# Kernel optimization log

Measured on AMD Instinct MI355X. Metric: run time of the kernel, lower is better.

## Reference

```python
import jax, jax.numpy as jnp
import numpy as np

ROUTINGS = 3
NUM_CAPSULE = 32
DIM_CAPSULE = 32
EPS_KERAS = 1e-7   # K.epsilon()
EPS_L2 = 1e-12     # tf.nn.l2_normalize epsilon


def squash(x, axis=-1):
    s2 = jnp.sum(jnp.square(x), axis=axis, keepdims=True)
    return (s2 / (1.0 + s2)) * x / jnp.sqrt(s2 + EPS_KERAS)


def l2_normalize(x, axis=-1):
    s2 = jnp.sum(jnp.square(x), axis=axis, keepdims=True)
    return x * jax.lax.rsqrt(jnp.maximum(s2, EPS_L2))


def setup_inputs() -> dict:
    key = jax.random.key(0)
    k1, k2 = jax.random.split(key)
    u_vecs = jax.random.normal(k1, (32, 2048, 16), dtype=jnp.float32)
    # glorot-like small scale for the local kernel to keep routing numerics sane
    W = jax.random.normal(k2, (2048, 16, NUM_CAPSULE * DIM_CAPSULE), dtype=jnp.float32) * 0.05
    return {"u_vecs": u_vecs, "W": W}


def reference(u_vecs, W):
    B, N_in, _ = u_vecs.shape
    # local_conv1d with kernel size 1 == per-input-capsule matmul
    u_hat = jnp.einsum('bni,nio->bno', u_vecs, W)
    # [B, N_in, num_cap, dim] -> [B, num_cap, N_in, dim]
    u_hat = u_hat.reshape(B, N_in, NUM_CAPSULE, DIM_CAPSULE).transpose(0, 2, 1, 3)
    b = jnp.zeros((B, NUM_CAPSULE, N_in), dtype=u_hat.dtype)
    o = None
    for i in range(ROUTINGS):
        c = jax.nn.softmax(b, axis=1)              # softmax over output capsules
        o = jnp.einsum('bin,binj->bij', c, u_hat)  # [B, num_cap, dim]
        if i < ROUTINGS - 1:
            o = l2_normalize(o, axis=-1)
            b = jnp.einsum('bij,binj->bin', o, u_hat)
    return squash(o, axis=-1)
```

## Files before the change

### kernel.cpp

```cpp
#include <hip/hip_runtime.h>
#include <math.h>
#include <stdint.h>

#define BB   32
#define NN   2048
#define KK   16
#define CC   32
#define DD   32
#define NCOL 1024
#define NPB  8
#define WT   (KK * NCOL)
#define OSZ  (BB * NCOL)
#define NGRP (NN / NPB)
#define NSLICE 8

__global__ __launch_bounds__(512) __attribute__((amdgpu_waves_per_eu(2)))
void caps_stage(const float* __restrict__ u, const float* __restrict__ W,
                const float* __restrict__ onorm, float* __restrict__ part)
{
    __shared__ float ush[NPB * KK * BB];

    const int tid  = threadIdx.x;
    const int wv   = tid >> 6;
    const int lane = tid & 63;
    const int oct  = lane >> 3;
    const int dq   = lane & 7;
    const int b0   = wv << 2;
    const int n0   = blockIdx.x * NPB;

    for (int idx = tid; idx < NPB * KK * BB; idx += 512) {
        const int k = idx & 15, b = (idx >> 4) & 31, n = idx >> 9;
        ush[(n << 9) + (k << 5) + b] =
            u[(size_t)b * (NN * KK) + (size_t)(n0 + n) * KK + k];
    }
    __syncthreads();

    const float* wp = W + (size_t)n0 * WT + (lane << 2);

    float opart[4][4][4];
#pragma unroll
    for (int b = 0; b < 4; ++b)
#pragma unroll
        for (int j = 0; j < 4; ++j)
#pragma unroll
            for (int e = 0; e < 4; ++e) opart[b][j][e] = 0.f;

    for (int nn = 0; nn < NPB; ++nn) {
        const float* un = &ush[nn << 9];

        float accU[4][4][4];
#pragma unroll
        for (int b = 0; b < 4; ++b)
#pragma unroll
            for (int j = 0; j < 4; ++j)
#pragma unroll
                for (int e = 0; e < 4; ++e) accU[b][j][e] = 0.f;

#pragma unroll
        for (int k = 0; k < KK; ++k) {
            const float4 w0 = *(const float4*)(wp + k * NCOL);
            const float4 w1 = *(const float4*)(wp + k * NCOL + 256);
            const float4 w2 = *(const float4*)(wp + k * NCOL + 512);
            const float4 w3 = *(const float4*)(wp + k * NCOL + 768);
            const float4 ub = *(const float4*)&un[(k << 5) + b0];
            const float us[4] = {ub.x, ub.y, ub.z, ub.w};
#pragma unroll
            for (int b = 0; b < 4; ++b) {
                accU[b][0][0] = fmaf(us[b], w0.x, accU[b][0][0]);
                accU[b][0][1] = fmaf(us[b], w0.y, accU[b][0][1]);
                accU[b][0][2] = fmaf(us[b], w0.z, accU[b][0][2]);
                accU[b][0][3] = fmaf(us[b], w0.w, accU[b][0][3]);
                accU[b][1][0] = fmaf(us[b], w1.x, accU[b][1][0]);
                accU[b][1][1] = fmaf(us[b], w1.y, accU[b][1][1]);
                accU[b][1][2] = fmaf(us[b], w1.z, accU[b][1][2]);
                accU[b][1][3] = fmaf(us[b], w1.w, accU[b][1][3]);
                accU[b][2][0] = fmaf(us[b], w2.x, accU[b][2][0]);
                accU[b][2][1] = fmaf(us[b], w2.y, accU[b][2][1]);
                accU[b][2][2] = fmaf(us[b], w2.z, accU[b][2][2]);
                accU[b][2][3] = fmaf(us[b], w2.w, accU[b][2][3]);
                accU[b][3][0] = fmaf(us[b], w3.x, accU[b][3][0]);
                accU[b][3][1] = fmaf(us[b], w3.y, accU[b][3][1]);
                accU[b][3][2] = fmaf(us[b], w3.z, accU[b][3][2]);
                accU[b][3][3] = fmaf(us[b], w3.w, accU[b][3][3]);
            }
        }
        wp += WT;

        float cv[4][4];
#pragma unroll
        for (int b = 0; b < 4; ++b) {
            float L[4];
#pragma unroll
            for (int j = 0; j < 4; ++j) {
                const float4 on4 = *(const float4*)(
                    onorm + ((size_t)(b0 + b) * CC + oct + (j << 3)) * DD + (dq << 2));
                float p = accU[b][j][0] * on4.x + accU[b][j][1] * on4.y
                        + accU[b][j][2] * on4.z + accU[b][j][3] * on4.w;
                p += __shfl_xor(p, 1);
                p += __shfl_xor(p, 2);
                p += __shfl_xor(p, 4);
                L[j] = p;
            }
            float mx = fmaxf(fmaxf(L[0], L[1]), fmaxf(L[2], L[3]));
            mx = fmaxf(mx, __shfl_xor(mx, 8));
            mx = fmaxf(mx, __shfl_xor(mx, 16));
            mx = fmaxf(mx, __shfl_xor(mx, 32));
            float s = 0.f;
#pragma unroll
            for (int j = 0; j < 4; ++j) { L[j] = __expf(L[j] - mx); s += L[j]; }
            s += __shfl_xor(s, 8);
            s += __shfl_xor(s, 16);
            s += __shfl_xor(s, 32);
            const float inv = 1.f / s;
#pragma unroll
            for (int j = 0; j < 4; ++j) cv[b][j] = L[j] * inv;
        }

#pragma unroll
        for (int b = 0; b < 4; ++b)
#pragma unroll
            for (int j = 0; j < 4; ++j)
#pragma unroll
                for (int e = 0; e < 4; ++e)
                    opart[b][j][e] = fmaf(cv[b][j], accU[b][j][e], opart[b][j][e]);
    }

    float* my = part + (size_t)blockIdx.x * OSZ + (size_t)b0 * NCOL + (lane << 2);
#pragma unroll
    for (int b = 0; b < 4; ++b)
#pragma unroll
        for (int j = 0; j < 4; ++j) {
            float4 v;
            v.x = opart[b][j][0]; v.y = opart[b][j][1];
            v.z = opart[b][j][2]; v.w = opart[b][j][3];
            *(float4*)&my[b * NCOL + (j << 8)] = v;
        }
}

__global__ __launch_bounds__(256) void caps_reduce1(
    const float* __restrict__ part, float* __restrict__ ws2)
{
    const int gid   = blockIdx.x * 256 + threadIdx.x;
    const int slice = gid >> 13;
    const int q     = gid & 8191;
    float4 acc = make_float4(0.f, 0.f, 0.f, 0.f);
    const float* p = part + ((size_t)slice * 32) * OSZ + (q << 2);
#pragma unroll 8
    for (int j = 0; j < 32; ++j) {
        const float4 v = *(const float4*)(p + (size_t)j * OSZ);
        acc.x += v.x; acc.y += v.y; acc.z += v.z; acc.w += v.w;
    }
    *(float4*)(ws2 + ((size_t)gid << 2)) = acc;
}

__global__ __launch_bounds__(256) void caps_reduce2(
    const float* __restrict__ ws2, float* __restrict__ dst, int mode)
{
    const int q = blockIdx.x * 256 + threadIdx.x;
    float4 acc = make_float4(0.f, 0.f, 0.f, 0.f);
#pragma unroll
    for (int s = 0; s < NSLICE; ++s) {
        const float4 v = *(const float4*)(ws2 + ((size_t)s << 15) + (q << 2));
        acc.x += v.x; acc.y += v.y; acc.z += v.z; acc.w += v.w;
    }
    float s2 = acc.x * acc.x + acc.y * acc.y + acc.z * acc.z + acc.w * acc.w;
    s2 += __shfl_xor(s2, 1);
    s2 += __shfl_xor(s2, 2);
    s2 += __shfl_xor(s2, 4);
    float scale;
    if (mode == 0) {
        scale = rsqrtf(fmaxf(s2, 1e-12f));
    } else {
        scale = (s2 / (1.f + s2)) / sqrtf(s2 + 1e-7f);
    }
    float4 o;
    o.x = acc.x * scale; o.y = acc.y * scale;
    o.z = acc.z * scale; o.w = acc.w * scale;
    *(float4*)(dst + ((size_t)q << 2)) = o;
}

extern "C" void kernel_launch(void* const* d_in, const int* in_sizes, int n_in,
                              void* d_out, int out_size, void* d_ws, size_t ws_size,
                              hipStream_t stream)
{
    const float* u = (const float*)d_in[0];
    const float* W = (const float*)d_in[1];
    float* out = (float*)d_out;

    float* part  = (float*)d_ws;
    float* ws2   = part + (size_t)NGRP * OSZ;
    float* onorm = ws2 + (size_t)NSLICE * OSZ;

    hipMemsetAsync(onorm, 0, (size_t)OSZ * sizeof(float), stream);

    for (int it = 0; it < 3; ++it) {
        caps_stage<<<NGRP, 512, 0, stream>>>(u, W, onorm, part);
        caps_reduce1<<<256, 256, 0, stream>>>(part, ws2);
        if (it < 2)
            caps_reduce2<<<32, 256, 0, stream>>>(ws2, onorm, 0);
        else
            caps_reduce2<<<32, 256, 0, stream>>>(ws2, out, 1);
    }
}
```

Measured before the change: 410.6 us.

## Split batch across two block halves to double grid size in caps stage

```diff
diff --git a/kernel.cpp b/kernel.cpp
--- a/kernel.cpp
+++ b/kernel.cpp
@@ -3,6 +3,7 @@
 #include <stdint.h>
 
 #define BB   32
+#define HB   16
 #define NN   2048
 #define KK   16
 #define CC   32
@@ -13,44 +14,49 @@
 #define OSZ  (BB * NCOL)
 #define NGRP (NN / NPB)
 #define NSLICE 8
+#define KP   17
 
 __global__ __launch_bounds__(512) __attribute__((amdgpu_waves_per_eu(2)))
 void caps_stage(const float* __restrict__ u, const float* __restrict__ W,
                 const float* __restrict__ onorm, float* __restrict__ part)
 {
-    __shared__ float ush[NPB * KK * BB];
+    __shared__ float ush[NPB * KK * KP];
 
     const int tid  = threadIdx.x;
     const int wv   = tid >> 6;
     const int lane = tid & 63;
     const int oct  = lane >> 3;
     const int dq   = lane & 7;
-    const int b0   = wv << 2;
-    const int n0   = blockIdx.x * NPB;
-
-    for (int idx = tid; idx < NPB * KK * BB; idx += 512) {
-        const int k = idx & 15, b = (idx >> 4) & 31, n = idx >> 9;
-        ush[(n << 9) + (k << 5) + b] =
-            u[(size_t)b * (NN * KK) + (size_t)(n0 + n) * KK + k];
+    const int b0   = wv << 1;
+
+    const int ngrp  = blockIdx.x & 255;
+    const int bhalf = blockIdx.x >> 8;
+    const int n0    = ngrp * NPB;
+    const int bbase = bhalf * HB;
+
+    for (int idx = tid; idx < NPB * KK * HB; idx += 512) {
+        const int k = idx & 15, b = (idx >> 4) & 15, n = idx >> 8;
+        ush[n * (KK * KP) + k * KP + b] =
+            u[(size_t)(bbase + b) * (NN * KK) + (size_t)(n0 + n) * KK + k];
     }
     __syncthreads();
 
     const float* wp = W + (size_t)n0 * WT + (lane << 2);
 
-    float opart[4][4][4];
-#pragma unroll
-    for (int b = 0; b < 4; ++b)
+    float opart[2][4][4];
+#pragma unroll
+    for (int b = 0; b < 2; ++b)
 #pragma unroll
         for (int j = 0; j < 4; ++j)
 #pragma unroll
             for (int e = 0; e < 4; ++e) opart[b][j][e] = 0.f;
 
     for (int nn = 0; nn < NPB; ++nn) {
-        const float* un = &ush[nn << 9];
-
-        float accU[4][4][4];
-#pragma unroll
-        for (int b = 0; b < 4; ++b)
+        const float* un = &ush[nn * (KK * KP)];
+
+        float accU[2][4][4];
+#pragma unroll
+        for (int b = 0; b < 2; ++b)
 #pragma unroll
             for (int j = 0; j < 4; ++j)
 #pragma unroll
@@ -62,10 +68,11 @@
             const float4 w1 = *(const float4*)(wp + k * NCOL + 256);
             const float4 w2 = *(const float4*)(wp + k * NCOL + 512);
             const float4 w3 = *(const float4*)(wp + k * NCOL + 768);
-            const float4 ub = *(const float4*)&un[(k << 5) + b0];
-            const float us[4] = {ub.x, ub.y, ub.z, ub.w};
-#pragma unroll
-            for (int b = 0; b < 4; ++b) {
+            const float u0 = un[k * KP + b0];
+            const float u1 = un[k * KP + b0 + 1];
+            const float us[2] = {u0, u1};
+#pragma unroll
+            for (int b = 0; b < 2; ++b) {
                 accU[b][0][0] = fmaf(us[b], w0.x, accU[b][0][0]);
                 accU[b][0][1] = fmaf(us[b], w0.y, accU[b][0][1]);
                 accU[b][0][2] = fmaf(us[b], w0.z, accU[b][0][2]);
@@ -86,14 +93,15 @@
         }
         wp += WT;
 
-        float cv[4][4];
-#pragma unroll
-        for (int b = 0; b < 4; ++b) {
+        float cv[2][4];
+#pragma unroll
+        for (int b = 0; b < 2; ++b) {
+            const int gb = bbase + b0 + b;
             float L[4];
 #pragma unroll
             for (int j = 0; j < 4; ++j) {
                 const float4 on4 = *(const float4*)(
-                    onorm + ((size_t)(b0 + b) * CC + oct + (j << 3)) * DD + (dq << 2));
+                    onorm + ((size_t)gb * CC + oct + (j << 3)) * DD + (dq << 2));
                 float p = accU[b][j][0] * on4.x + accU[b][j][1] * on4.y
                         + accU[b][j][2] * on4.z + accU[b][j][3] * on4.w;
                 p += __shfl_xor(p, 1);
@@ -117,7 +125,7 @@
         }
 
 #pragma unroll
-        for (int b = 0; b < 4; ++b)
+        for (int b = 0; b < 2; ++b)
 #pragma unroll
             for (int j = 0; j < 4; ++j)
 #pragma unroll
@@ -125,9 +133,10 @@
                     opart[b][j][e] = fmaf(cv[b][j], accU[b][j][e], opart[b][j][e]);
     }
 
-    float* my = part + (size_t)blockIdx.x * OSZ + (size_t)b0 * NCOL + (lane << 2);
-#pragma unroll
-    for (int b = 0; b < 4; ++b)
+    float* my = part + (size_t)ngrp * OSZ
+              + (size_t)(bbase + b0) * NCOL + (lane << 2);
+#pragma unroll
+    for (int b = 0; b < 2; ++b)
 #pragma unroll
         for (int j = 0; j < 4; ++j) {
             float4 v;
@@ -194,7 +203,7 @@
     hipMemsetAsync(onorm, 0, (size_t)OSZ * sizeof(float), stream);
 
     for (int it = 0; it < 3; ++it) {
-        caps_stage<<<NGRP, 512, 0, stream>>>(u, W, onorm, part);
+        caps_stage<<<2 * NGRP, 512, 0, stream>>>(u, W, onorm, part);
         caps_reduce1<<<256, 256, 0, stream>>>(part, ws2);
         if (it < 2)
             caps_reduce2<<<32, 256, 0, stream>>>(ws2, onorm, 0);
```

New measurement: 968.4 us. +135.9%, slower.
